# Performance work log

Hardware: AMD Instinct MI355X
Metric: run time of the kernel (lower is better)

Reference implementation:

```python
import jax, jax.numpy as jnp
import numpy as np

B, C, H, W = 4, 256, 64, 64
N = H * W


def setup_inputs() -> dict:
    key = jax.random.key(0)
    k1, k2, k3, k4, k5 = jax.random.split(key, 5)
    energy = jax.random.normal(k1, (B, N, N), dtype=jnp.float32)
    x = jax.random.normal(k2, (B, C, H, W), dtype=jnp.float32)
    # 1x1 conv params (kernel is [C_out, C_in] after squeezing the 1x1 spatial dims)
    fan = 1.0 / np.sqrt(C)
    value_w = jax.random.uniform(k3, (C, C), dtype=jnp.float32, minval=-fan, maxval=fan)
    value_b = jax.random.uniform(k4, (C,), dtype=jnp.float32, minval=-fan, maxval=fan)
    # nn.Parameter(torch.zeros(1)) -> use small random scalar so output is non-trivial
    gamma = jax.random.normal(k5, (1,), dtype=jnp.float32) * 0.1
    return {"energy": energy, "x": x, "value_w": value_w, "value_b": value_b, "gamma": gamma}


def reference(energy, x, value_w, value_b, gamma):
    # softmax over last dim of the [B, N, N] score matrix (dropout in eval mode = identity)
    attention = jax.nn.softmax(energy, axis=-1)  # [B, N, N]
    # 1x1 conv: per-pixel channel mixing
    value = jnp.einsum('bchw,oc->bohw', x, value_w) + value_b[None, :, None, None]
    value = value.reshape(x.shape[0], -1, N)  # [B, C, N]
    # out[b,c,m] = sum_n value[b,c,n] * attention[b,m,n]  (bmm with attention^T)
    out = jnp.einsum('bcn,bmn->bcm', value, attention)
    out = out.reshape(x.shape)  # [B, C, H, W]
    return gamma[0] * out + 2.0 * x
```

## Files before the change

### kernel.cpp

```cpp
#include <hip/hip_runtime.h>

#define Nn 4096
#define Cc 256
#define NN2 ((size_t)Nn * Nn)

typedef __attribute__((ext_vector_type(8))) short bf16x8;
typedef __attribute__((ext_vector_type(4))) short bf16x4;
typedef __attribute__((ext_vector_type(4))) float f32x4;

#define GLOAD(src, dst) __builtin_amdgcn_global_load_lds( \
    (const __attribute__((address_space(1))) void*)(src), \
    (__attribute__((address_space(3))) void*)(dst), 16, 0, 0)

__device__ __forceinline__ unsigned short f2bf(float f) {
    union { float f; unsigned u; } v; v.f = f;
    unsigned r = v.u + 0x7FFF + ((v.u >> 16) & 1);
    return (unsigned short)(r >> 16);
}

__device__ __forceinline__ bf16x8 pack2(const float4& a, const float4& b) {
    bf16x8 o;
    o[0] = (short)f2bf(a.x); o[1] = (short)f2bf(a.y);
    o[2] = (short)f2bf(a.z); o[3] = (short)f2bf(a.w);
    o[4] = (short)f2bf(b.x); o[5] = (short)f2bf(b.y);
    o[6] = (short)f2bf(b.z); o[7] = (short)f2bf(b.w);
    return o;
}

__device__ __forceinline__ void expstore4(const float4& a,
                                          unsigned short* dst, float& sacc) {
    const float s0 = __expf(a.x), s1 = __expf(a.y), s2 = __expf(a.z), s3 = __expf(a.w);
    sacc += (s0 + s1) + (s2 + s3);
    bf16x4 o;
    o[0] = (short)f2bf(s0); o[1] = (short)f2bf(s1);
    o[2] = (short)f2bf(s2); o[3] = (short)f2bf(s3);
    *(bf16x4*)dst = o;
}

__global__ __launch_bounds__(256) void value_gemm(
    const float* __restrict__ X, const float* __restrict__ W,
    const float* __restrict__ bias, unsigned short* __restrict__ Vout)
{
    __shared__ float Xs[256][33];

    const int t = threadIdx.x;
    const int b  = blockIdx.x >> 7;
    const int n0 = (blockIdx.x & 127) << 5;
    const int wave = t >> 6, lane = t & 63;
    const int lrow = lane & 15, lq = lane >> 4;

    const float* Xb = X + (size_t)b * Cc * Nn + n0;

    {
        const int r0 = t >> 3, c4 = (t & 7) << 2;
        #pragma unroll
        for (int i = 0; i < 8; ++i) {
            const int r = r0 + i * 32;
            const float4 v = *(const float4*)(Xb + (size_t)r * Nn + c4);
            Xs[r][c4 + 0] = v.x; Xs[r][c4 + 1] = v.y;
            Xs[r][c4 + 2] = v.z; Xs[r][c4 + 3] = v.w;
        }
    }
    __syncthreads();

    f32x4 acc[4][2] = {};

    #pragma unroll 2
    for (int k0 = 0; k0 < Cc; k0 += 32) {
        bf16x8 af[4];
        #pragma unroll
        for (int ci = 0; ci < 4; ++ci) {
            const float* wp = W + (size_t)(wave * 64 + ci * 16 + lrow) * Cc + k0 + lq * 8;
            af[ci] = pack2(*(const float4*)wp, *(const float4*)(wp + 4));
        }
        bf16x8 bp[2];
        #pragma unroll
        for (int mi = 0; mi < 2; ++mi) {
            const int n = mi * 16 + lrow;
            bf16x8 o;
            #pragma unroll
            for (int j = 0; j < 8; ++j) o[j] = (short)f2bf(Xs[k0 + lq * 8 + j][n]);
            bp[mi] = o;
        }
        #pragma unroll
        for (int ci = 0; ci < 4; ++ci)
            #pragma unroll
            for (int mi = 0; mi < 2; ++mi)
                acc[ci][mi] = __builtin_amdgcn_mfma_f32_16x16x32_bf16(
                    af[ci], bp[mi], acc[ci][mi], 0, 0, 0);
    }

    #pragma unroll
    for (int ci = 0; ci < 4; ++ci) {
        #pragma unroll
        for (int rr = 0; rr < 4; ++rr) {
            const int o = wave * 64 + ci * 16 + lq * 4 + rr;
            const float bo = bias[o];
            #pragma unroll
            for (int mi = 0; mi < 2; ++mi) {
                const int n = n0 + mi * 16 + lrow;
                Vout[((size_t)(b * Cc + o)) * Nn + n] = f2bf(acc[ci][mi][rr] + bo);
            }
        }
    }
}

__global__ __launch_bounds__(512, 4) void attn_gemm(
    const unsigned short* __restrict__ V, const float* __restrict__ E,
    const float* __restrict__ X, const float* __restrict__ gamma,
    float* __restrict__ Out)
{
    __shared__ float Eraw[4][32 * 64];
    __shared__ unsigned short Bexp[2][32 * 64];
    __shared__ float sum_lds[32];

    const int t = threadIdx.x;
    const int wave = t >> 6, lane = t & 63;
    const int lrow = lane & 15, lq = lane >> 4;
    const int l7 = lrow & 7;
    const int blk = blockIdx.x;
    const int b  = (blk & 7) >> 1;
    const int m0 = (((blk >> 3) << 1) | (blk & 1)) << 5;

    const int erow = t >> 4, eg = t & 15;
    const int eslot = erow * 64 + eg * 4;
    const int ss = erow * 64 + (((eg >> 1) ^ (erow & 7)) << 3) + ((eg & 1) << 2);

    const int drow = wave * 4 + (lane >> 4);
    const float* egbase = E + (size_t)b * NN2 + (size_t)(m0 + drow) * Nn + ((lane & 15) << 2);

    const unsigned short* vbase = V + (size_t)(b * Cc + wave * 32) * Nn;
    const int voff0 = lrow * Nn + lq * 8;
    const int voff1 = (16 + lrow) * Nn + lq * 8;

    f32x4 acc[2][2] = {};
    float sacc = 0.f;
    bf16x8 vA[4], vB[4];

    GLOAD(egbase,            &Eraw[0][wave * 256]);
    GLOAD(egbase + (1 << 6), &Eraw[1][wave * 256]);
    GLOAD(egbase + (2 << 6), &Eraw[2][wave * 256]);
    vA[0] = *(const bf16x8*)(vbase + voff0);
    vA[1] = *(const bf16x8*)(vbase + voff1);
    vA[2] = *(const bf16x8*)(vbase + voff0 + 32);
    vA[3] = *(const bf16x8*)(vbase + voff1 + 32);
    asm volatile("s_waitcnt vmcnt(6)" ::: "memory");
    __builtin_amdgcn_s_barrier();
    {
        const float4 ev = *(const float4*)&Eraw[0][eslot];
        expstore4(ev, &Bexp[0][ss], sacc);
    }

#define STEP(T, Vc, Vn, DO_DMA, DO_EXP, DO_VL, VMC)                            \
    {                                                                          \
        asm volatile("s_waitcnt lgkmcnt(0)" ::: "memory");                     \
        __builtin_amdgcn_s_barrier();                                          \
        if (DO_VL) {                                                           \
            const int kv = ((T) + 1) << 6;                                     \
            Vn[0] = *(const bf16x8*)(vbase + voff0 + kv);                      \
            Vn[1] = *(const bf16x8*)(vbase + voff1 + kv);                      \
            Vn[2] = *(const bf16x8*)(vbase + voff0 + kv + 32);                 \
            Vn[3] = *(const bf16x8*)(vbase + voff1 + kv + 32);                 \
        }                                                                      \
        if (DO_DMA) {                                                          \
            GLOAD(egbase + (((T) + 3) << 6), &Eraw[((T) + 3) & 3][wave * 256]);\
        }                                                                      \
        bf16x8 bfr[2][2];                                                      \
        _Pragma("unroll")                                                      \
        for (int kk = 0; kk < 2; ++kk)                                         \
            _Pragma("unroll")                                                  \
            for (int mi = 0; mi < 2; ++mi) {                                   \
                const int rm = mi * 16 + lrow;                                 \
                bfr[kk][mi] = *(const bf16x8*)                                 \
                    &Bexp[(T) & 1][rm * 64 + (((kk * 4 + lq) ^ l7) << 3)];     \
            }                                                                  \
        asm volatile("s_waitcnt vmcnt(" #VMC ")" ::: "memory");                \
        if (DO_EXP) {                                                          \
            const float4 ev = *(const float4*)&Eraw[((T) + 1) & 3][eslot];     \
            expstore4(ev, &Bexp[((T) + 1) & 1][ss], sacc);                     \
        }                                                                      \
        __builtin_amdgcn_s_setprio(1);                                         \
        _Pragma("unroll")                                                      \
        for (int ci = 0; ci < 2; ++ci)                                         \
            _Pragma("unroll")                                                  \
            for (int mi = 0; mi < 2; ++mi) {                                   \
                acc[ci][mi] = __builtin_amdgcn_mfma_f32_16x16x32_bf16(         \
                    Vc[0 * 2 + ci], bfr[0][mi], acc[ci][mi], 0, 0, 0);         \
                acc[ci][mi] = __builtin_amdgcn_mfma_f32_16x16x32_bf16(         \
                    Vc[1 * 2 + ci], bfr[1][mi], acc[ci][mi], 0, 0, 0);         \
            }                                                                  \
        __builtin_amdgcn_s_setprio(0);                                         \
    }

    #pragma unroll 1
    for (int k = 0; k < 60; k += 2) {
        STEP(k,     vA, vB, 1, 1, 1, 6);
        STEP(k + 1, vB, vA, 1, 1, 1, 6);
    }
    STEP(60, vA, vB, 1, 1, 1, 6);
    STEP(61, vB, vA, 0, 1, 1, 0);
    STEP(62, vA, vB, 0, 1, 1, 0);
    STEP(63, vB, vA, 0, 0, 0, 0);
#undef STEP

    {
        float s = sacc;
        s += __shfl_xor(s, 1);
        s += __shfl_xor(s, 2);
        s += __shfl_xor(s, 4);
        s += __shfl_xor(s, 8);
        if (eg == 0) sum_lds[erow] = s;
    }
    __syncthreads();

    const float g = gamma[0];
    #pragma unroll
    for (int mi = 0; mi < 2; ++mi) {
        const int mloc = mi * 16 + lrow;
        const float scale = g / sum_lds[mloc];
        const int m = m0 + mloc;
        #pragma unroll
        for (int ci = 0; ci < 2; ++ci) {
            #pragma unroll
            for (int rr = 0; rr < 4; ++rr) {
                const int c = wave * 32 + ci * 16 + lq * 4 + rr;
                const size_t off = ((size_t)(b * Cc + c)) * Nn + m;
                Out[off] = scale * acc[ci][mi][rr] + 2.0f * X[off];
            }
        }
    }
}

extern "C" void kernel_launch(void* const* d_in, const int* in_sizes, int n_in,
                              void* d_out, int out_size, void* d_ws, size_t ws_size,
                              hipStream_t stream) {
    const float* energy  = (const float*)d_in[0];
    const float* x       = (const float*)d_in[1];
    const float* value_w = (const float*)d_in[2];
    const float* value_b = (const float*)d_in[3];
    const float* gamma   = (const float*)d_in[4];
    float* out = (float*)d_out;
    unsigned short* Vws = (unsigned short*)d_ws;

    value_gemm<<<512, 256, 0, stream>>>(x, value_w, value_b, Vws);
    attn_gemm<<<512, 512, 0, stream>>>(Vws, energy, x, gamma, out);
}
```

Before: 455.5 us.

## Fuse value conv into attention kernel by reassociating W·(X·Aᵀ)

Drops the separate value-projection kernel. The fused kernel first computes Y = X·exp(E)ᵀ on raw X converted to bf16, then applies the 1x1 conv weight to Y from LDS afterwards. Because the softmax rows sum to one, the bias term collapses to gamma*bias. The block tile grows to 64 rows with half as many blocks, energy is loaded through registers instead of LDS DMA, and bf16 conversion uses the packed hardware instruction. The risks are lower occupancy from the large LDS footprint, and only 256 blocks on a chip with many CUs.

Result: slower. 480.5 us (+5.5%).

```diff
diff --git a/kernel.cpp b/kernel.cpp
--- a/kernel.cpp
+++ b/kernel.cpp
@@ -5,202 +5,123 @@
 #define NN2 ((size_t)Nn * Nn)
 
 typedef __attribute__((ext_vector_type(8))) short bf16x8;
-typedef __attribute__((ext_vector_type(4))) short bf16x4;
 typedef __attribute__((ext_vector_type(4))) float f32x4;
 
-#define GLOAD(src, dst) __builtin_amdgcn_global_load_lds( \
-    (const __attribute__((address_space(1))) void*)(src), \
-    (__attribute__((address_space(3))) void*)(dst), 16, 0, 0)
-
-__device__ __forceinline__ unsigned short f2bf(float f) {
-    union { float f; unsigned u; } v; v.f = f;
-    unsigned r = v.u + 0x7FFF + ((v.u >> 16) & 1);
-    return (unsigned short)(r >> 16);
-}
-
-__device__ __forceinline__ bf16x8 pack2(const float4& a, const float4& b) {
-    bf16x8 o;
-    o[0] = (short)f2bf(a.x); o[1] = (short)f2bf(a.y);
-    o[2] = (short)f2bf(a.z); o[3] = (short)f2bf(a.w);
-    o[4] = (short)f2bf(b.x); o[5] = (short)f2bf(b.y);
-    o[6] = (short)f2bf(b.z); o[7] = (short)f2bf(b.w);
-    return o;
-}
-
-__device__ __forceinline__ void expstore4(const float4& a,
+#define LDSBAR() do { \
+    asm volatile("s_waitcnt lgkmcnt(0)" ::: "memory"); \
+    __builtin_amdgcn_s_barrier(); \
+} while (0)
+
+__device__ __forceinline__ unsigned cvtpk(float lo, float hi) {
+    unsigned r;
+    asm("v_cvt_pk_bf16_f32 %0, %1, %2" : "=v"(r) : "v"(lo), "v"(hi));
+    return r;
+}
+
+__device__ __forceinline__ bf16x8 cvt8(const float4 a, const float4 b) {
+    union { unsigned u[4]; bf16x8 v; } o;
+    o.u[0] = cvtpk(a.x, a.y); o.u[1] = cvtpk(a.z, a.w);
+    o.u[2] = cvtpk(b.x, b.y); o.u[3] = cvtpk(b.z, b.w);
+    return o.v;
+}
+
+__device__ __forceinline__ void expstore8(const float4 a, const float4 b,
                                           unsigned short* dst, float& sacc) {
-    const float s0 = __expf(a.x), s1 = __expf(a.y), s2 = __expf(a.z), s3 = __expf(a.w);
-    sacc += (s0 + s1) + (s2 + s3);
-    bf16x4 o;
-    o[0] = (short)f2bf(s0); o[1] = (short)f2bf(s1);
-    o[2] = (short)f2bf(s2); o[3] = (short)f2bf(s3);
-    *(bf16x4*)dst = o;
-}
-
-__global__ __launch_bounds__(256) void value_gemm(
-    const float* __restrict__ X, const float* __restrict__ W,
-    const float* __restrict__ bias, unsigned short* __restrict__ Vout)
+    float4 ea, eb;
+    ea.x = __expf(a.x); ea.y = __expf(a.y); ea.z = __expf(a.z); ea.w = __expf(a.w);
+    eb.x = __expf(b.x); eb.y = __expf(b.y); eb.z = __expf(b.z); eb.w = __expf(b.w);
+    sacc += ((ea.x + ea.y) + (ea.z + ea.w)) + ((eb.x + eb.y) + (eb.z + eb.w));
+    *(bf16x8*)dst = cvt8(ea, eb);
+}
+
+__global__ __launch_bounds__(512) void fused_attn(
+    const float* __restrict__ E, const float* __restrict__ X,
+    const float* __restrict__ W, const float* __restrict__ bias,
+    const float* __restrict__ gamma, float* __restrict__ Out)
 {
-    __shared__ float Xs[256][33];
-
-    const int t = threadIdx.x;
-    const int b  = blockIdx.x >> 7;
-    const int n0 = (blockIdx.x & 127) << 5;
-    const int wave = t >> 6, lane = t & 63;
-    const int lrow = lane & 15, lq = lane >> 4;
-
-    const float* Xb = X + (size_t)b * Cc * Nn + n0;
-
-    {
-        const int r0 = t >> 3, c4 = (t & 7) << 2;
-        #pragma unroll
-        for (int i = 0; i < 8; ++i) {
-            const int r = r0 + i * 32;
-            const float4 v = *(const float4*)(Xb + (size_t)r * Nn + c4);
-            Xs[r][c4 + 0] = v.x; Xs[r][c4 + 1] = v.y;
-            Xs[r][c4 + 2] = v.z; Xs[r][c4 + 3] = v.w;
-        }
-    }
-    __syncthreads();
-
-    f32x4 acc[4][2] = {};
-
-    #pragma unroll 2
-    for (int k0 = 0; k0 < Cc; k0 += 32) {
-        bf16x8 af[4];
-        #pragma unroll
-        for (int ci = 0; ci < 4; ++ci) {
-            const float* wp = W + (size_t)(wave * 64 + ci * 16 + lrow) * Cc + k0 + lq * 8;
-            af[ci] = pack2(*(const float4*)wp, *(const float4*)(wp + 4));
-        }
-        bf16x8 bp[2];
-        #pragma unroll
-        for (int mi = 0; mi < 2; ++mi) {
-            const int n = mi * 16 + lrow;
-            bf16x8 o;
-            #pragma unroll
-            for (int j = 0; j < 8; ++j) o[j] = (short)f2bf(Xs[k0 + lq * 8 + j][n]);
-            bp[mi] = o;
-        }
-        #pragma unroll
-        for (int ci = 0; ci < 4; ++ci)
-            #pragma unroll
-            for (int mi = 0; mi < 2; ++mi)
-                acc[ci][mi] = __builtin_amdgcn_mfma_f32_16x16x32_bf16(
-                    af[ci], bp[mi], acc[ci][mi], 0, 0, 0);
-    }
-
-    #pragma unroll
-    for (int ci = 0; ci < 4; ++ci) {
-        #pragma unroll
-        for (int rr = 0; rr < 4; ++rr) {
-            const int o = wave * 64 + ci * 16 + lq * 4 + rr;
-            const float bo = bias[o];
-            #pragma unroll
-            for (int mi = 0; mi < 2; ++mi) {
-                const int n = n0 + mi * 16 + lrow;
-                Vout[((size_t)(b * Cc + o)) * Nn + n] = f2bf(acc[ci][mi][rr] + bo);
-            }
-        }
-    }
-}
-
-__global__ __launch_bounds__(512, 4) void attn_gemm(
-    const unsigned short* __restrict__ V, const float* __restrict__ E,
-    const float* __restrict__ X, const float* __restrict__ gamma,
-    float* __restrict__ Out)
-{
-    __shared__ float Eraw[4][32 * 64];
-    __shared__ unsigned short Bexp[2][32 * 64];
-    __shared__ float sum_lds[32];
+    __shared__ unsigned short Bexp[2][64 * 64];
+    __shared__ unsigned short Ylds[64 * 256];
+    __shared__ float sum_lds[64];
 
     const int t = threadIdx.x;
     const int wave = t >> 6, lane = t & 63;
     const int lrow = lane & 15, lq = lane >> 4;
-    const int l7 = lrow & 7;
     const int blk = blockIdx.x;
     const int b  = (blk & 7) >> 1;
-    const int m0 = (((blk >> 3) << 1) | (blk & 1)) << 5;
-
-    const int erow = t >> 4, eg = t & 15;
-    const int eslot = erow * 64 + eg * 4;
-    const int ss = erow * 64 + (((eg >> 1) ^ (erow & 7)) << 3) + ((eg & 1) << 2);
-
-    const int drow = wave * 4 + (lane >> 4);
-    const float* egbase = E + (size_t)b * NN2 + (size_t)(m0 + drow) * Nn + ((lane & 15) << 2);
-
-    const unsigned short* vbase = V + (size_t)(b * Cc + wave * 32) * Nn;
-    const int voff0 = lrow * Nn + lq * 8;
-    const int voff1 = (16 + lrow) * Nn + lq * 8;
-
-    f32x4 acc[2][2] = {};
+    const int m0 = (((blk >> 3) << 1) | (blk & 1)) << 6;
+    const int q0 = wave << 5;
+
+    const int erow = t >> 3, eg = t & 7;
+    const float* ep = E + (size_t)b * NN2 + (size_t)(m0 + erow) * Nn + eg * 8;
+    unsigned short* const bst0 = &Bexp[0][erow * 64 + ((eg ^ (erow & 7)) << 3)];
+    unsigned short* const bst1 = &Bexp[1][erow * 64 + ((eg ^ (erow & 7)) << 3)];
+
+    const float* xp0 = X + (size_t)b * Cc * Nn + (size_t)(q0 + lrow) * Nn + lq * 8;
+    const float* xp1 = xp0 + (size_t)16 * Nn;
+
+    f32x4 acc[2][4] = {};
     float sacc = 0.f;
-    bf16x8 vA[4], vB[4];
-
-    GLOAD(egbase,            &Eraw[0][wave * 256]);
-    GLOAD(egbase + (1 << 6), &Eraw[1][wave * 256]);
-    GLOAD(egbase + (2 << 6), &Eraw[2][wave * 256]);
-    vA[0] = *(const bf16x8*)(vbase + voff0);
-    vA[1] = *(const bf16x8*)(vbase + voff1);
-    vA[2] = *(const bf16x8*)(vbase + voff0 + 32);
-    vA[3] = *(const bf16x8*)(vbase + voff1 + 32);
-    asm volatile("s_waitcnt vmcnt(6)" ::: "memory");
-    __builtin_amdgcn_s_barrier();
-    {
-        const float4 ev = *(const float4*)&Eraw[0][eslot];
-        expstore4(ev, &Bexp[0][ss], sacc);
-    }
-
-#define STEP(T, Vc, Vn, DO_DMA, DO_EXP, DO_VL, VMC)                            \
+
+    float4 e0a, e0b, e1a, e1b;
+    bf16x8 xA[4], xB[4];
+
+    e0a = *(const float4*)(ep);       e0b = *(const float4*)(ep + 4);
+    e1a = *(const float4*)(ep + 64);  e1b = *(const float4*)(ep + 68);
+    #pragma unroll
+    for (int kk = 0; kk < 2; ++kk) {
+        xA[kk * 2 + 0] = cvt8(*(const float4*)(xp0 + kk * 32),
+                              *(const float4*)(xp0 + kk * 32 + 4));
+        xA[kk * 2 + 1] = cvt8(*(const float4*)(xp1 + kk * 32),
+                              *(const float4*)(xp1 + kk * 32 + 4));
+    }
+    expstore8(e0a, e0b, bst0, sacc);
+    e0a = *(const float4*)(ep + 128); e0b = *(const float4*)(ep + 132);
+    LDSBAR();
+
+#define STEP(K, Xc, Xn, Ea, Eb, LAST)                                          \
     {                                                                          \
-        asm volatile("s_waitcnt lgkmcnt(0)" ::: "memory");                     \
-        __builtin_amdgcn_s_barrier();                                          \
-        if (DO_VL) {                                                           \
-            const int kv = ((T) + 1) << 6;                                     \
-            Vn[0] = *(const bf16x8*)(vbase + voff0 + kv);                      \
-            Vn[1] = *(const bf16x8*)(vbase + voff1 + kv);                      \
-            Vn[2] = *(const bf16x8*)(vbase + voff0 + kv + 32);                 \
-            Vn[3] = *(const bf16x8*)(vbase + voff1 + kv + 32);                 \
-        }                                                                      \
-        if (DO_DMA) {                                                          \
-            GLOAD(egbase + (((T) + 3) << 6), &Eraw[((T) + 3) & 3][wave * 256]);\
-        }                                                                      \
-        bf16x8 bfr[2][2];                                                      \
-        _Pragma("unroll")                                                      \
-        for (int kk = 0; kk < 2; ++kk)                                         \
+        if (!(LAST)) {                                                         \
+            const int kx = ((K) + 1) << 6;                                     \
             _Pragma("unroll")                                                  \
-            for (int mi = 0; mi < 2; ++mi) {                                   \
-                const int rm = mi * 16 + lrow;                                 \
-                bfr[kk][mi] = *(const bf16x8*)                                 \
-                    &Bexp[(T) & 1][rm * 64 + (((kk * 4 + lq) ^ l7) << 3)];     \
+            for (int kk = 0; kk < 2; ++kk) {                                   \
+                Xn[kk * 2 + 0] = cvt8(*(const float4*)(xp0 + kx + kk * 32),    \
+                                      *(const float4*)(xp0 + kx + kk * 32 + 4));\
+                Xn[kk * 2 + 1] = cvt8(*(const float4*)(xp1 + kx + kk * 32),    \
+                                      *(const float4*)(xp1 + kx + kk * 32 + 4));\
             }                                                                  \
-        asm volatile("s_waitcnt vmcnt(" #VMC ")" ::: "memory");                \
-        if (DO_EXP) {                                                          \
-            const float4 ev = *(const float4*)&Eraw[((T) + 1) & 3][eslot];     \
-            expstore4(ev, &Bexp[((T) + 1) & 1][ss], sacc);                     \
+            expstore8(Ea, Eb, ((K) & 1) ? bst0 : bst1, sacc);                  \
+            const int ke = (((K) + 3) & 63) << 6;                              \
+            Ea = *(const float4*)(ep + ke);                                    \
+            Eb = *(const float4*)(ep + ke + 4);                                \
         }                                                                      \
         __builtin_amdgcn_s_setprio(1);                                         \
         _Pragma("unroll")                                                      \
-        for (int ci = 0; ci < 2; ++ci)                                         \
-            _Pragma("unroll")                                                  \
-            for (int mi = 0; mi < 2; ++mi) {                                   \
-                acc[ci][mi] = __builtin_amdgcn_mfma_f32_16x16x32_bf16(         \
-                    Vc[0 * 2 + ci], bfr[0][mi], acc[ci][mi], 0, 0, 0);         \
-                acc[ci][mi] = __builtin_amdgcn_mfma_f32_16x16x32_bf16(         \
-                    Vc[1 * 2 + ci], bfr[1][mi], acc[ci][mi], 0, 0, 0);         \
-            }                                                                  \
+        for (int mi = 0; mi < 4; ++mi) {                                       \
+            const int rm = mi * 16 + lrow;                                     \
+            const bf16x8 f0 = *(const bf16x8*)                                 \
+                &Bexp[(K) & 1][rm * 64 + ((lq ^ (rm & 7)) << 3)];              \
+            const bf16x8 f1 = *(const bf16x8*)                                 \
+                &Bexp[(K) & 1][rm * 64 + (((4 + lq) ^ (rm & 7)) << 3)];        \
+            acc[0][mi] = __builtin_amdgcn_mfma_f32_16x16x32_bf16(              \
+                Xc[0], f0, acc[0][mi], 0, 0, 0);                               \
+            acc[1][mi] = __builtin_amdgcn_mfma_f32_16x16x32_bf16(              \
+                Xc[1], f0, acc[1][mi], 0, 0, 0);                               \
+            acc[0][mi] = __builtin_amdgcn_mfma_f32_16x16x32_bf16(              \
+                Xc[2], f1, acc[0][mi], 0, 0, 0);                               \
+            acc[1][mi] = __builtin_amdgcn_mfma_f32_16x16x32_bf16(              \
+                Xc[3], f1, acc[1][mi], 0, 0, 0);                               \
+        }                                                                      \
         __builtin_amdgcn_s_setprio(0);                                         \
+        LDSBAR();                                                              \
     }
 
     #pragma unroll 1
-    for (int k = 0; k < 60; k += 2) {
-        STEP(k,     vA, vB, 1, 1, 1, 6);
-        STEP(k + 1, vB, vA, 1, 1, 1, 6);
-    }
-    STEP(60, vA, vB, 1, 1, 1, 6);
-    STEP(61, vB, vA, 0, 1, 1, 0);
-    STEP(62, vA, vB, 0, 1, 1, 0);
-    STEP(63, vB, vA, 0, 0, 0, 0);
+    for (int k = 0; k < 62; k += 2) {
+        STEP(k,     xA, xB, e1a, e1b, 0);
+        STEP(k + 1, xB, xA, e0a, e0b, 0);
+    }
+    STEP(62, xA, xB, e1a, e1b, 0);
+    STEP(63, xB, xA, e0a, e0b, 1);
 #undef STEP
 
     {
@@ -208,14 +129,49 @@
         s += __shfl_xor(s, 1);
         s += __shfl_xor(s, 2);
         s += __shfl_xor(s, 4);
-        s += __shfl_xor(s, 8);
         if (eg == 0) sum_lds[erow] = s;
     }
+
+    #pragma unroll
+    for (int ci = 0; ci < 2; ++ci) {
+        #pragma unroll
+        for (int mi = 0; mi < 4; ++mi) {
+            const int m = mi * 16 + lrow;
+            const int q = q0 + ci * 16 + lq * 4;
+            const unsigned u0 = cvtpk(acc[ci][mi][0], acc[ci][mi][1]);
+            const unsigned u1 = cvtpk(acc[ci][mi][2], acc[ci][mi][3]);
+            unsigned short* dst =
+                &Ylds[m * 256 + ((((q >> 3) ^ (m & 7)) << 3) | (q & 7))];
+            *(unsigned long long*)dst =
+                (unsigned long long)u0 | ((unsigned long long)u1 << 32);
+        }
+    }
     __syncthreads();
 
+    f32x4 a2[2][4] = {};
+    const float* wp0 = W + (size_t)(q0 + lrow) * Cc + lq * 8;
+    const float* wp1 = wp0 + (size_t)16 * Cc;
+    #pragma unroll
+    for (int kq = 0; kq < 8; ++kq) {
+        const bf16x8 wf0 = cvt8(*(const float4*)(wp0 + kq * 32),
+                                *(const float4*)(wp0 + kq * 32 + 4));
+        const bf16x8 wf1 = cvt8(*(const float4*)(wp1 + kq * 32),
+                                *(const float4*)(wp1 + kq * 32 + 4));
+        #pragma unroll
+        for (int mi = 0; mi < 4; ++mi) {
+            const int m = mi * 16 + lrow;
+            const bf16x8 yf = *(const bf16x8*)
+                &Ylds[m * 256 + ((((kq * 4 + lq) ^ (m & 7)) << 3))];
+            a2[0][mi] = __builtin_amdgcn_mfma_f32_16x16x32_bf16(
+                wf0, yf, a2[0][mi], 0, 0, 0);
+            a2[1][mi] = __builtin_amdgcn_mfma_f32_16x16x32_bf16(
+                wf1, yf, a2[1][mi], 0, 0, 0);
+        }
+    }
+
     const float g = gamma[0];
     #pragma unroll
-    for (int mi = 0; mi < 2; ++mi) {
+    for (int mi = 0; mi < 4; ++mi) {
         const int mloc = mi * 16 + lrow;
         const float scale = g / sum_lds[mloc];
         const int m = m0 + mloc;
@@ -223,9 +179,9 @@
         for (int ci = 0; ci < 2; ++ci) {
             #pragma unroll
             for (int rr = 0; rr < 4; ++rr) {
-                const int c = wave * 32 + ci * 16 + lq * 4 + rr;
+                const int c = q0 + ci * 16 + lq * 4 + rr;
                 const size_t off = ((size_t)(b * Cc + c)) * Nn + m;
-                Out[off] = scale * acc[ci][mi][rr] + 2.0f * X[off];
+                Out[off] = scale * a2[ci][mi][rr] + g * bias[c] + 2.0f * X[off];
             }
         }
     }
@@ -240,8 +196,7 @@
     const float* value_b = (const float*)d_in[3];
     const float* gamma   = (const float*)d_in[4];
     float* out = (float*)d_out;
-    unsigned short* Vws = (unsigned short*)d_ws;
-
-    value_gemm<<<512, 256, 0, stream>>>(x, value_w, value_b, Vws);
-    attn_gemm<<<512, 512, 0, stream>>>(Vws, energy, x, gamma, out);
-}
+    (void)d_ws; (void)ws_size;
+
+    fused_attn<<<256, 512, 0, stream>>>(energy, x, value_w, value_b, gamma, out);
+}
```
